# Optimization experiments

Hardware: AMD Instinct MI355X
Metric: run time of the kernel (lower is better)

Reference implementation:

```python
import jax, jax.numpy as jnp
import numpy as np

WS = 8          # window size M
SHIFT = WS // 2 # cyclic shift
HEADS = 8


def _rel_pos_index(ws):
    # (ws*ws, ws*ws) indices into the (2ws-1)^2 bias table
    coords = np.stack(np.meshgrid(np.arange(ws), np.arange(ws), indexing='ij'), 0).reshape(2, -1)
    rel = coords[:, :, None] - coords[:, None, :]          # (2, N, N)
    rel = rel.transpose(1, 2, 0) + (ws - 1)                # shift to [0, 2ws-2]
    return rel[..., 0] * (2 * ws - 1) + rel[..., 1]        # (N, N)


def _shift_mask(H, W, ws, shift):
    # standard Swin attention mask for shifted windows: (nWin, N, N)
    img = np.zeros((H, W), dtype=np.int32)
    cnt = 0
    for hs in (slice(0, -ws), slice(-ws, -shift), slice(-shift, None)):
        for wsl in (slice(0, -ws), slice(-ws, -shift), slice(-shift, None)):
            img[hs, wsl] = cnt
            cnt += 1
    mw = img.reshape(H // ws, ws, W // ws, ws).transpose(0, 2, 1, 3).reshape(-1, ws * ws)
    diff = mw[:, None, :] - mw[:, :, None]
    return np.where(diff != 0, -100.0, 0.0).astype(np.float32)


def setup_inputs() -> dict:
    key = jax.random.key(0)
    ks = jax.random.split(key, 6)
    B, C, H, W = 32, 256, 64, 64
    return {
        'x': jax.random.normal(ks[0], (B, C, H, W), jnp.float32),
        'w_qkv': jax.random.normal(ks[1], (C, 3 * C), jnp.float32) * (C ** -0.5),
        'b_qkv': jnp.zeros((3 * C,), jnp.float32),
        'w_o': jax.random.normal(ks[2], (C, C), jnp.float32) * (C ** -0.5),
        'b_o': jnp.zeros((C,), jnp.float32),
        'rel_bias_table': jax.random.normal(ks[3], ((2 * WS - 1) ** 2, HEADS), jnp.float32) * 0.02,
    }


def reference(x, w_qkv, b_qkv, w_o, b_o, rel_bias_table):
    B, C, H, W = x.shape
    ws, shift, heads = WS, SHIFT, HEADS
    dh = C // heads
    nH, nW = H // ws, W // ws
    nWin, N = nH * nW, ws * ws

    rel_idx = jnp.asarray(_rel_pos_index(ws))                 # (N, N) int
    mask = jnp.asarray(_shift_mask(H, W, ws, shift))          # (nWin, N, N)

    # cyclic shift
    xs = jnp.roll(x, (-shift, -shift), axis=(2, 3))
    # window partition: (B, C, H, W) -> (B, nWin, N, C)
    xw = xs.reshape(B, C, nH, ws, nW, ws).transpose(0, 2, 4, 3, 5, 1).reshape(B, nWin, N, C)

    qkv = xw @ w_qkv + b_qkv                                  # (B, nWin, N, 3C)
    qkv = qkv.reshape(B, nWin, N, 3, heads, dh)
    q = qkv[..., 0, :, :].transpose(0, 1, 3, 2, 4)            # (B, nWin, h, N, dh)
    k = qkv[..., 1, :, :].transpose(0, 1, 3, 2, 4)
    v = qkv[..., 2, :, :].transpose(0, 1, 3, 2, 4)

    attn = jnp.einsum('bwhnd,bwhmd->bwhnm', q, k) * (dh ** -0.5)
    bias = rel_bias_table[rel_idx]                            # (N, N, heads)
    attn = attn + bias.transpose(2, 0, 1)[None, None]         # add rel pos bias
    attn = attn + mask[None, :, None]                         # add shift mask
    attn = jax.nn.softmax(attn, axis=-1)

    out = jnp.einsum('bwhnm,bwhmd->bwhnd', attn, v)           # (B, nWin, h, N, dh)
    out = out.transpose(0, 1, 3, 2, 4).reshape(B, nWin, N, C)
    out = out @ w_o + b_o

    # window reverse: (B, nWin, N, C) -> (B, C, H, W)
    out = out.reshape(B, nH, nW, ws, ws, C).transpose(0, 5, 1, 3, 2, 4).reshape(B, C, H, W)
    # reverse cyclic shift
    return jnp.roll(out, (shift, shift), axis=(2, 3))
```

## Files before the change

### kernel.cpp

```cpp
#include <hip/hip_runtime.h>
#include <stdint.h>

typedef __attribute__((ext_vector_type(8))) short short8;
typedef __attribute__((ext_vector_type(4))) float floatx4;
typedef unsigned short u16;
typedef unsigned int u32;

#define MFMA16(a,b,c) __builtin_amdgcn_mfma_f32_16x16x32_bf16((a),(b),(c),0,0,0)

__device__ __forceinline__ u16 f2b(float f){
  u32 i; __builtin_memcpy(&i,&f,4); i += 0x7FFFu + ((i>>16)&1u); return (u16)(i>>16);
}
__device__ __forceinline__ int regid(int p){ return (p<56)?0:((p<60)?1:2); }

#define SCO 16896
#define LDS_ELEMS 26112

__global__ void prep_w(const float* __restrict__ wqkv, const float* __restrict__ wo,
                       u16* __restrict__ wqkvT, u16* __restrict__ woT){
  int idx = blockIdx.x*256 + threadIdx.x;
  if(idx < 768*256){ int n = idx>>8, k = idx&255; wqkvT[idx] = f2b(wqkv[k*768 + n]); }
  else { int j = idx - 768*256; int n = j>>8, k = j&255; woT[j] = f2b(wo[k*256 + n]); }
}

__global__ __launch_bounds__(256,3) void swmsa_fused(
    const float* __restrict__ x, const u16* __restrict__ wqkvT, const float* __restrict__ bqkv,
    const u16* __restrict__ woT, const float* __restrict__ bo, const float* __restrict__ table,
    float* __restrict__ out)
{
  extern __shared__ u16 lds[];
  const int tid  = threadIdx.x;
  const int wave = tid>>6, lane = tid&63;
  const int quad = lane>>4, colid = lane&15;
  const int bi = blockIdx.x;
  const int xcd = bi & 7, j = bi >> 3;
  const int r0 = ((j >> 3) << 3) | xcd;
  const int wx = j & 7;
  const int b = r0 >> 3, wy = r0 & 7;
  const size_t imgbase = (size_t)b*256*4096;
  const int w0 = wx*8+4;
  const floatx4 fzero = {0.f,0.f,0.f,0.f};
  u16* sc = lds + SCO + wave*2304;

  for(int i=0;i<2;++i){
    int unit = tid + 256*i;
    int cg = unit>>3, ty = unit&7;
    int hs = (wy*8+ty+4)&63;
    u16 vv[4][8];
    #pragma unroll
    for(int cc=0;cc<4;++cc){
      const float* src = x + imgbase + (size_t)(cg*4+cc)*4096 + (size_t)hs*64;
      floatx4 lo, hi;
      if(wx<7){ lo = *(const floatx4*)(src+w0); hi = *(const floatx4*)(src+w0+4); }
      else    { lo = *(const floatx4*)(src+60); hi = *(const floatx4*)(src); }
      #pragma unroll
      for(int t=0;t<4;++t){ vv[cc][t]=f2b(lo[t]); vv[cc][4+t]=f2b(hi[t]); }
    }
    #pragma unroll
    for(int t=0;t<8;++t){
      uint64_t pk = (uint64_t)vv[0][t] | ((uint64_t)vv[1][t]<<16)
                  | ((uint64_t)vv[2][t]<<32) | ((uint64_t)vv[3][t]<<48);
      *(uint64_t*)&lds[(ty*8+t)*264 + cg*4] = pk;
    }
  }
  __syncthreads();

  short8 aq2[2][4], bk2[2][4], bv2[2][2][2];
  for(int t3=0; t3<3; ++t3){
    const int cc = 2 - t3;
    const int col0 = (cc*4 + wave)*64;
    floatx4 acc[4][4];
    #pragma unroll
    for(int mt=0;mt<4;++mt)
      #pragma unroll
      for(int nt=0;nt<4;++nt) acc[mt][nt] = fzero;
    for(int k0=0;k0<256;k0+=32){
      short8 af[4], bfr[4];
      #pragma unroll
      for(int mt=0;mt<4;++mt) af[mt]  = *(const short8*)&lds[(mt*16+colid)*264 + k0 + quad*8];
      #pragma unroll
      for(int nt=0;nt<4;++nt) bfr[nt] = *(const short8*)&wqkvT[(size_t)(col0+nt*16+colid)*256 + k0 + quad*8];
      #pragma unroll
      for(int mt=0;mt<4;++mt)
        #pragma unroll
        for(int nt=0;nt<4;++nt) acc[mt][nt] = MFMA16(af[mt], bfr[nt], acc[mt][nt]);
    }
    #pragma unroll
    for(int hf=0; hf<2; ++hf){
      #pragma unroll
      for(int nt2=0; nt2<2; ++nt2){
        int nt = hf*2 + nt2;
        float bias = bqkv[col0 + nt*16 + colid];
        #pragma unroll
        for(int mt=0;mt<4;++mt)
          #pragma unroll
          for(int rr=0;rr<4;++rr){
            int row = mt*16 + quad*4 + rr;
            u16 bvv = f2b(acc[mt][nt][rr] + bias);
            if(cc==2) sc[(nt2*16+colid)*72 + row] = bvv;
            else      sc[row*36 + nt2*16 + colid] = bvv;
          }
      }
      if(cc==2){
        #pragma unroll
        for(int n2=0;n2<2;++n2)
          #pragma unroll
          for(int kc=0;kc<2;++kc)
            bv2[hf][n2][kc] = *(const short8*)&sc[(n2*16+colid)*72 + kc*32 + quad*8];
      } else if(cc==1){
        #pragma unroll
        for(int mt=0;mt<4;++mt) bk2[hf][mt] = *(const short8*)&sc[(mt*16+colid)*36 + quad*8];
      } else {
        #pragma unroll
        for(int mt=0;mt<4;++mt) aq2[hf][mt] = *(const short8*)&sc[(mt*16+colid)*36 + quad*8];
      }
    }
  }
  __syncthreads();

  const float scale = 0.17677669529663687f;
  #pragma unroll
  for(int hi=0; hi<2; ++hi){
    const int h = wave*2 + hi;
    floatx4 s[4][4];
    #pragma unroll
    for(int mt=0;mt<4;++mt)
      #pragma unroll
      for(int nt=0;nt<4;++nt) s[mt][nt] = MFMA16(aq2[hi][mt], bk2[hi][nt], fzero);
    int cntk[4], kys[4], kxs[4];
    #pragma unroll
    for(int nt=0;nt<4;++nt){
      int col = nt*16 + colid;
      kys[nt] = col>>3; kxs[nt] = col&7;
      cntk[nt] = regid(wy*8 + kys[nt])*3 + regid(wx*8 + kxs[nt]);
    }
    #pragma unroll
    for(int mt=0;mt<4;++mt)
      #pragma unroll
      for(int rr=0;rr<4;++rr){
        int row = mt*16 + quad*4 + rr;
        int ty = row>>3, tx = row&7;
        int cntq = regid(wy*8+ty)*3 + regid(wx*8+tx);
        #pragma unroll
        for(int nt=0;nt<4;++nt){
          int rel = (ty - kys[nt] + 7)*15 + (tx - kxs[nt] + 7);
          float add = table[rel*8 + h] + ((cntq==cntk[nt]) ? 0.f : -100.f);
          s[mt][nt][rr] = s[mt][nt][rr]*scale + add;
        }
      }
    u32 gpk[4][4];
    #pragma unroll
    for(int mt=0;mt<4;++mt)
      #pragma unroll
      for(int rr=0;rr<4;++rr){
        float mx = s[mt][0][rr];
        #pragma unroll
        for(int nt=1;nt<4;++nt) mx = fmaxf(mx, s[mt][nt][rr]);
        #pragma unroll
        for(int d=1; d<16; d<<=1) mx = fmaxf(mx, __shfl_xor(mx, d));
        float e[4], sum = 0.f;
        #pragma unroll
        for(int nt=0;nt<4;++nt){ e[nt] = __expf(s[mt][nt][rr]-mx); sum += e[nt]; }
        #pragma unroll
        for(int d=1; d<16; d<<=1) sum += __shfl_xor(sum, d);
        float inv = 1.0f/sum;
        int row = mt*16 + quad*4 + rr;
        sc[row*36 + colid]      = f2b(e[0]*inv);
        sc[row*36 + 16 + colid] = f2b(e[1]*inv);
        gpk[mt][rr] = (u32)f2b(e[2]*inv) | ((u32)f2b(e[3]*inv) << 16);
      }
    floatx4 o[4][2];
    #pragma unroll
    for(int mt=0;mt<4;++mt){ o[mt][0]=fzero; o[mt][1]=fzero; }
    #pragma unroll
    for(int kc=0;kc<2;++kc){
      if(kc==1){
        #pragma unroll
        for(int mt=0;mt<4;++mt)
          #pragma unroll
          for(int rr=0;rr<4;++rr){
            int row = mt*16 + quad*4 + rr;
            sc[row*36 + colid]      = (u16)(gpk[mt][rr] & 0xffffu);
            sc[row*36 + 16 + colid] = (u16)(gpk[mt][rr] >> 16);
          }
      }
      short8 ap[4];
      #pragma unroll
      for(int mt=0;mt<4;++mt) ap[mt] = *(const short8*)&sc[(mt*16+colid)*36 + quad*8];
      #pragma unroll
      for(int mt=0;mt<4;++mt)
        #pragma unroll
        for(int n2=0;n2<2;++n2) o[mt][n2] = MFMA16(ap[mt], bv2[hi][n2][kc], o[mt][n2]);
    }
    #pragma unroll
    for(int n2=0;n2<2;++n2){
      int c = h*32 + n2*16 + colid;
      #pragma unroll
      for(int mt=0;mt<4;++mt)
        #pragma unroll
        for(int rr=0;rr<4;++rr)
          lds[(mt*16+quad*4+rr)*264 + c] = f2b(o[mt][n2][rr]);
    }
  }
  __syncthreads();

  float* oQ = (float*)(lds + SCO);
  for(int np=0; np<4; ++np){
    const int col0 = np*64 + wave*16;
    floatx4 acc[4];
    #pragma unroll
    for(int mt=0;mt<4;++mt) acc[mt] = fzero;
    for(int k0=0;k0<256;k0+=32){
      short8 ay[4], bw;
      #pragma unroll
      for(int mt=0;mt<4;++mt) ay[mt] = *(const short8*)&lds[(mt*16+colid)*264 + k0 + quad*8];
      bw = *(const short8*)&woT[(size_t)(col0+colid)*256 + k0 + quad*8];
      #pragma unroll
      for(int mt=0;mt<4;++mt) acc[mt] = MFMA16(ay[mt], bw, acc[mt]);
    }
    if(np) __syncthreads();
    {
      float bias = bo[col0 + colid];
      int cl = wave*16 + colid;
      #pragma unroll
      for(int mt=0;mt<4;++mt)
        #pragma unroll
        for(int rr=0;rr<4;++rr)
          oQ[cl*72 + mt*16 + quad*4 + rr] = acc[mt][rr] + bias;
    }
    __syncthreads();
    #pragma unroll
    for(int i=0;i<2;++i){
      int unit = tid + 256*i;
      int cl = unit>>3, ty = unit&7;
      floatx4 lo  = *(const floatx4*)&oQ[cl*72 + ty*8];
      floatx4 hi2 = *(const floatx4*)&oQ[cl*72 + ty*8 + 4];
      int hd = (wy*8+ty+4)&63;
      float* dst = out + imgbase + (size_t)(np*64+cl)*4096 + (size_t)hd*64;
      if(wx<7){ *(floatx4*)(dst+w0) = lo; *(floatx4*)(dst+w0+4) = hi2; }
      else    { *(floatx4*)(dst+60) = lo; *(floatx4*)(dst)      = hi2; }
    }
  }
}

extern "C" void kernel_launch(void* const* d_in, const int* in_sizes, int n_in,
                              void* d_out, int out_size, void* d_ws, size_t ws_size,
                              hipStream_t stream) {
  const float* x     = (const float*)d_in[0];
  const float* wqkv  = (const float*)d_in[1];
  const float* bqkv  = (const float*)d_in[2];
  const float* wo    = (const float*)d_in[3];
  const float* bo    = (const float*)d_in[4];
  const float* table = (const float*)d_in[5];
  float* out = (float*)d_out;

  u16* wqkvT = (u16*)d_ws;
  u16* woT   = wqkvT + 768*256;

  prep_w<<<1024, 256, 0, stream>>>(wqkv, wo, wqkvT, woT);

  (void)hipFuncSetAttribute((const void*)swmsa_fused,
                            hipFuncAttributeMaxDynamicSharedMemorySize, LDS_ELEMS*2);
  swmsa_fused<<<2048, 256, LDS_ELEMS*2, stream>>>(x, wqkvT, bqkv, woT, bo, table, out);
}
```

Baseline: 483.6 us.

## Prefetch QKV weight fragments and write output projection directly to global

In the QKV projection loop, the weight fragments for the next k-step are loaded one iteration ahead (double-buffered registers), so global load latency can overlap with the MFMAs. The output projection now keeps all four column-block accumulators in registers and stores each accumulator fragment straight to global memory with its bias added. This removes the LDS staging buffer and the per-block __syncthreads. The cost is higher register pressure (64 accumulator floats plus prefetch buffers), which can lower occupancy, and global stores of 16 bytes per lane instead of staged coalesced rows.

```diff
diff --git a/kernel.cpp b/kernel.cpp
--- a/kernel.cpp
+++ b/kernel.cpp
@@ -69,21 +69,29 @@
   for(int t3=0; t3<3; ++t3){
     const int cc = 2 - t3;
     const int col0 = (cc*4 + wave)*64;
+    const u16* wslab = wqkvT + (size_t)(col0+colid)*256 + quad*8;
     floatx4 acc[4][4];
     #pragma unroll
     for(int mt=0;mt<4;++mt)
       #pragma unroll
       for(int nt=0;nt<4;++nt) acc[mt][nt] = fzero;
+    short8 bcur[4], bnxt[4];
+    #pragma unroll
+    for(int nt=0;nt<4;++nt) bcur[nt] = *(const short8*)&wslab[(size_t)nt*16*256];
     for(int k0=0;k0<256;k0+=32){
-      short8 af[4], bfr[4];
+      short8 af[4];
       #pragma unroll
       for(int mt=0;mt<4;++mt) af[mt]  = *(const short8*)&lds[(mt*16+colid)*264 + k0 + quad*8];
-      #pragma unroll
-      for(int nt=0;nt<4;++nt) bfr[nt] = *(const short8*)&wqkvT[(size_t)(col0+nt*16+colid)*256 + k0 + quad*8];
+      if(k0 < 224){
+        #pragma unroll
+        for(int nt=0;nt<4;++nt) bnxt[nt] = *(const short8*)&wslab[(size_t)nt*16*256 + k0 + 32];
+      }
       #pragma unroll
       for(int mt=0;mt<4;++mt)
         #pragma unroll
-        for(int nt=0;nt<4;++nt) acc[mt][nt] = MFMA16(af[mt], bfr[nt], acc[mt][nt]);
+        for(int nt=0;nt<4;++nt) acc[mt][nt] = MFMA16(af[mt], bcur[nt], acc[mt][nt]);
+      #pragma unroll
+      for(int nt=0;nt<4;++nt) bcur[nt] = bnxt[nt];
     }
     #pragma unroll
     for(int hf=0; hf<2; ++hf){
@@ -204,41 +212,39 @@
   }
   __syncthreads();
 
-  float* oQ = (float*)(lds + SCO);
-  for(int np=0; np<4; ++np){
-    const int col0 = np*64 + wave*16;
-    floatx4 acc[4];
-    #pragma unroll
-    for(int mt=0;mt<4;++mt) acc[mt] = fzero;
+  {
+    floatx4 acc[4][4];
+    #pragma unroll
+    for(int np=0;np<4;++np)
+      #pragma unroll
+      for(int mt=0;mt<4;++mt) acc[np][mt] = fzero;
+    const u16* wbase = woT + (size_t)(wave*16+colid)*256 + quad*8;
     for(int k0=0;k0<256;k0+=32){
-      short8 ay[4], bw;
+      short8 ay[4];
       #pragma unroll
       for(int mt=0;mt<4;++mt) ay[mt] = *(const short8*)&lds[(mt*16+colid)*264 + k0 + quad*8];
-      bw = *(const short8*)&woT[(size_t)(col0+colid)*256 + k0 + quad*8];
-      #pragma unroll
-      for(int mt=0;mt<4;++mt) acc[mt] = MFMA16(ay[mt], bw, acc[mt]);
-    }
-    if(np) __syncthreads();
-    {
-      float bias = bo[col0 + colid];
-      int cl = wave*16 + colid;
-      #pragma unroll
-      for(int mt=0;mt<4;++mt)
-        #pragma unroll
-        for(int rr=0;rr<4;++rr)
-          oQ[cl*72 + mt*16 + quad*4 + rr] = acc[mt][rr] + bias;
-    }
-    __syncthreads();
-    #pragma unroll
-    for(int i=0;i<2;++i){
-      int unit = tid + 256*i;
-      int cl = unit>>3, ty = unit&7;
-      floatx4 lo  = *(const floatx4*)&oQ[cl*72 + ty*8];
-      floatx4 hi2 = *(const floatx4*)&oQ[cl*72 + ty*8 + 4];
-      int hd = (wy*8+ty+4)&63;
-      float* dst = out + imgbase + (size_t)(np*64+cl)*4096 + (size_t)hd*64;
-      if(wx<7){ *(floatx4*)(dst+w0) = lo; *(floatx4*)(dst+w0+4) = hi2; }
-      else    { *(floatx4*)(dst+60) = lo; *(floatx4*)(dst)      = hi2; }
+      #pragma unroll
+      for(int np=0;np<4;++np){
+        short8 bw = *(const short8*)&wbase[(size_t)np*16384 + k0];
+        #pragma unroll
+        for(int mt=0;mt<4;++mt) acc[np][mt] = MFMA16(ay[mt], bw, acc[np][mt]);
+      }
+    }
+    const int ty_base = quad>>1, txg = quad&1;
+    const int col = (wx<7) ? (w0 + 4*txg) : (txg ? 0 : 60);
+    #pragma unroll
+    for(int np=0;np<4;++np){
+      const int ch = np*64 + wave*16 + colid;
+      const float bias = bo[ch];
+      float* chbase = out + imgbase + (size_t)ch*4096;
+      #pragma unroll
+      for(int mt=0;mt<4;++mt){
+        int ty = 2*mt + ty_base;
+        int hd = (wy*8 + ty + 4) & 63;
+        floatx4 vsto = acc[np][mt];
+        vsto[0]+=bias; vsto[1]+=bias; vsto[2]+=bias; vsto[3]+=bias;
+        *(floatx4*)(chbase + (size_t)hd*64 + col) = vsto;
+      }
     }
   }
 }
```

Measured after the change: 479.3 us. About the same (-0.9%).
